# Performance work log

Hardware: AMD Instinct MI355X
Metric: run time of the kernel (lower is better)

## Reference

```python
import jax, jax.numpy as jnp
import numpy as np

N_NODES = 200_000
N_EDGES = 6_400_000
N_GRAPHS = 1024
F_IN = 16
H1 = 8
H2 = 16
STEPS = 4


def setup_inputs() -> dict:
    key = jax.random.key(0)
    ks = jax.random.split(key, 16)
    x = jax.random.normal(ks[0], (N_NODES, F_IN), jnp.float32)
    edge_index = jax.random.randint(ks[1], (2, N_EDGES), 0, N_NODES, dtype=jnp.int64)
    batch = jnp.sort(jax.random.randint(ks[2], (N_NODES,), 0, N_GRAPHS, dtype=jnp.int64))

    def p(k, shape):
        return jax.random.normal(k, shape, jnp.float32) * 0.1

    return {
        "x": x, "edge_index": edge_index, "batch": batch,
        # SAGEConv1: lin_l (neighbors, with bias) + lin_r (root, no bias)
        "W1l": p(ks[3], (H1, F_IN)), "b1l": jnp.zeros((H1,), jnp.float32), "W1r": p(ks[4], (H1, F_IN)),
        # SAGEConv2
        "W2l": p(ks[5], (H2, H1)), "b2l": jnp.zeros((H2,), jnp.float32), "W2r": p(ks[6], (H2, H1)),
        # Set2Set LSTM: input 2*H2, hidden H2, torch gate order (i, f, g, o)
        "Wih": p(ks[7], (4 * H2, 2 * H2)), "Whh": p(ks[8], (4 * H2, H2)),
        "bih": jnp.zeros((4 * H2,), jnp.float32), "bhh": jnp.zeros((4 * H2,), jnp.float32),
        # Final fc: 2*H2 -> 2
        "Wfc": p(ks[9], (2, 2 * H2)), "bfc": jnp.zeros((2,), jnp.float32),
    }


def _sage_conv(x, src, dst, Wl, bl, Wr):
    # PyG SAGEConv (mean aggr): out = lin_l(mean_j x_j) + lin_r(x_i)
    n = x.shape[0]
    agg = jax.ops.segment_sum(x[src], dst, num_segments=n)          # [N, F]
    deg = jax.ops.segment_sum(jnp.ones_like(dst, dtype=x.dtype), dst, num_segments=n)
    agg = agg / jnp.maximum(deg, 1.0)[:, None]
    return agg @ Wl.T + bl + x @ Wr.T


def _set2set(x, batch, Wih, Whh, bih, bhh):
    # order-invariant pooling with iterative content attention
    B = N_GRAPHS
    h = jnp.zeros((B, H2), x.dtype)
    c = jnp.zeros((B, H2), x.dtype)
    q_star = jnp.zeros((B, 2 * H2), x.dtype)
    for _ in range(STEPS):
        gates = q_star @ Wih.T + bih + h @ Whh.T + bhh
        i, f, g, o = jnp.split(gates, 4, axis=-1)
        c = jax.nn.sigmoid(f) * c + jax.nn.sigmoid(i) * jnp.tanh(g)
        h = jax.nn.sigmoid(o) * jnp.tanh(c)
        q = h                                                      # [B, H2]
        e = jnp.sum(x * q[batch], axis=-1)                         # [N]
        emax = jax.ops.segment_max(e, batch, num_segments=B)
        a = jnp.exp(e - emax[batch])
        asum = jax.ops.segment_sum(a, batch, num_segments=B)
        a = a / asum[batch]                                        # segment softmax
        r = jax.ops.segment_sum(a[:, None] * x, batch, num_segments=B)  # [B, H2]
        q_star = jnp.concatenate([q, r], axis=-1)
    return q_star


def reference(x, edge_index, batch, W1l, b1l, W1r, W2l, b2l, W2r,
              Wih, Whh, bih, bhh, Wfc, bfc):
    src, dst = edge_index[0], edge_index[1]
    x = jax.nn.relu(_sage_conv(x, src, dst, W1l, b1l, W1r))
    x = jax.nn.relu(_sage_conv(x, src, dst, W2l, b2l, W2r))
    q_star = _set2set(x, batch, Wih, Whh, bih, bhh)
    return q_star @ Wfc.T + bfc
```

## Files before the change

### kernel.cpp

```cpp
#include <hip/hip_runtime.h>

#define N_NODES 200000
#define N_EDGES 6400000
#define N_GRAPHS 1024
#define F_IN 16
#define H1 8
#define H2 16
#define STEPS 4

#define NB 1024
#define BNODES 196
#define CAPB 7168
#define CAP 7680
#define SMAX 320
#define RPT 14
#define RPADD 200

typedef _Float16 half8 __attribute__((ext_vector_type(8)));

__global__ void k_y1(const float* __restrict__ x, const float* __restrict__ W1l,
                     _Float16* __restrict__ y1) {
    int n = blockIdx.x * blockDim.x + threadIdx.x;
    if (n >= N_NODES) return;
    float xv[F_IN];
#pragma unroll
    for (int k = 0; k < F_IN; k++) xv[k] = x[(long long)n * F_IN + k];
    half8 o;
#pragma unroll
    for (int j = 0; j < H1; j++) {
        float s = 0.f;
#pragma unroll
        for (int k = 0; k < F_IN; k++) s += W1l[j * F_IN + k] * xv[k];
        o[j] = (_Float16)s;
    }
    *(half8*)&y1[(long long)n * H1] = o;
}

#define FILL_T 16384
__global__ __launch_bounds__(1024) void k_bin_fill(const int* __restrict__ src,
                                                   const int* __restrict__ dst,
                                                   int* __restrict__ gcur,
                                                   unsigned int* __restrict__ grec) {
    __shared__ int scnt[NB];
    __shared__ int soff[NB];
    int tid = threadIdx.x;
    long long ebase = (long long)blockIdx.x * FILL_T;
    scnt[tid] = 0;
    __syncthreads();
    unsigned int rec[16];
    unsigned int meta[16];
#pragma unroll
    for (int u = 0; u < 16; u++) {
        long long e = ebase + (long long)u * 1024 + tid;
        if (e < N_EDGES) {
            int d = __builtin_nontemporal_load(dst + e);
            int s = __builtin_nontemporal_load(src + e);
            int b = d / BNODES;
            int dl = d - b * BNODES;
            rec[u] = ((unsigned int)s << 8) | (unsigned int)dl;
            int r = atomicAdd(&scnt[b], 1);
            meta[u] = ((unsigned int)b << 16) | (unsigned int)r;
        } else {
            meta[u] = 0xFFFFFFFFu;
        }
    }
    __syncthreads();
    {
        int c = scnt[tid];
        soff[tid] = c ? atomicAdd(&gcur[tid], c) : 0;
    }
    __syncthreads();
#pragma unroll
    for (int u = 0; u < 16; u++) {
        if (meta[u] != 0xFFFFFFFFu) {
            int b = meta[u] >> 16;
            unsigned int slot = (unsigned int)soff[b] + (meta[u] & 0xFFFFu);
            if (slot < CAPB) grec[(unsigned int)b * CAPB + slot] = rec[u];
        }
    }
}

__device__ __forceinline__ void block_scan_hist(const int* hist, int* start,
                                                int tid, int* wsum) {
    int v = (tid < BNODES) ? hist[tid] : 0;
    int lane = tid & 63, w = tid >> 6;
    int s = v;
#pragma unroll
    for (int off = 1; off < 64; off <<= 1) {
        int u = __shfl_up(s, off);
        if (lane >= off) s += u;
    }
    if (lane == 63) wsum[w] = s;
    __syncthreads();
    int base = 0;
    for (int i = 0; i < w; i++) base += wsum[i];
    s += base;
    if (tid < BNODES) start[tid] = s - v;
    if (tid == 511) start[BNODES] = s;
    __syncthreads();
}

__global__ __launch_bounds__(512) void k_conv1(
    const float* __restrict__ x, const _Float16* __restrict__ y1,
    const int* __restrict__ bcount, unsigned int* __restrict__ grec,
    int* __restrict__ growptr,
    const float* __restrict__ b1l, const float* __restrict__ W1r,
    _Float16* __restrict__ h1) {
    __shared__ int lsrc[CAP];
    __shared__ int hist[BNODES];
    __shared__ int start[BNODES + 1];
    __shared__ int wsum[8];
    int b = blockIdx.x, tid = threadIdx.x;
    int rs = b * CAPB;
    int cnt = bcount[b]; if (cnt > CAPB) cnt = CAPB;
    for (int j = tid; j < BNODES; j += 512) hist[j] = 0;
    __syncthreads();
    unsigned int rec[RPT];
#pragma unroll
    for (int u = 0; u < RPT; u++) {
        int idx = u * 512 + tid;
        if (idx < cnt) {
            rec[u] = __builtin_nontemporal_load(grec + rs + idx);
            atomicAdd(&hist[rec[u] & 255], 1);
        } else {
            rec[u] = 0xFFFFFFFFu;
        }
    }
    __syncthreads();
    block_scan_hist(hist, start, tid, wsum);
    for (int j = tid; j < BNODES; j += 512) hist[j] = 0;
    __syncthreads();
#pragma unroll
    for (int u = 0; u < RPT; u++) {
        if (rec[u] != 0xFFFFFFFFu) {
            int dl = rec[u] & 255;
            int k = atomicAdd(&hist[dl], 1);
            lsrc[start[dl] + k] = (int)(rec[u] >> 8);
        }
    }
    __syncthreads();
    for (int j = tid; j < cnt; j += 512) grec[rs + j] = (unsigned int)lsrc[j];
    if (tid <= BNODES) growptr[b * RPADD + tid] = start[tid];
    if (tid < 2 * BNODES) {
        int dl = tid >> 1, half = tid & 1;
        int n = b * BNODES + dl;
        int s0 = start[dl], s1 = start[dl + 1];
        int mid = s0 + ((s1 - s0) >> 1);
        int ga = half ? mid : s0;
        int gb = half ? s1 : mid;
        float acc[H1];
#pragma unroll
        for (int k = 0; k < H1; k++) acc[k] = 0.f;
        int e = ga;
        for (; e + 4 <= gb; e += 4) {
            int a0 = lsrc[e], a1 = lsrc[e + 1], a2 = lsrc[e + 2], a3 = lsrc[e + 3];
            half8 v0 = *(const half8*)&y1[(long long)a0 * H1];
            half8 v1 = *(const half8*)&y1[(long long)a1 * H1];
            half8 v2 = *(const half8*)&y1[(long long)a2 * H1];
            half8 v3 = *(const half8*)&y1[(long long)a3 * H1];
#pragma unroll
            for (int k = 0; k < H1; k++)
                acc[k] += ((float)v0[k] + (float)v1[k]) + ((float)v2[k] + (float)v3[k]);
        }
        for (; e < gb; e++) {
            half8 v = *(const half8*)&y1[(long long)lsrc[e] * H1];
#pragma unroll
            for (int k = 0; k < H1; k++) acc[k] += (float)v[k];
        }
#pragma unroll
        for (int k = 0; k < H1; k++) acc[k] += __shfl_xor(acc[k], 1);
        if (half == 0 && n < N_NODES) {
            float inv = 1.0f / fmaxf((float)(s1 - s0), 1.0f);
            float xv[F_IN];
#pragma unroll
            for (int k = 0; k < F_IN; k++) xv[k] = x[(long long)n * F_IN + k];
            half8 o;
#pragma unroll
            for (int j = 0; j < H1; j++) {
                float s = acc[j] * inv + b1l[j];
#pragma unroll
                for (int k = 0; k < F_IN; k++) s += W1r[j * F_IN + k] * xv[k];
                o[j] = (_Float16)fmaxf(s, 0.0f);
            }
            *(half8*)&h1[(long long)n * H1] = o;
        }
    }
}

__global__ __launch_bounds__(512) void k_conv2(
    const _Float16* __restrict__ h1,
    const unsigned int* __restrict__ gsorted, const int* __restrict__ growptr,
    const float* __restrict__ b2l, const float* __restrict__ W2l,
    const float* __restrict__ W2r, float* __restrict__ h2) {
    int b = blockIdx.x, tid = threadIdx.x;
    if (tid >= 2 * BNODES) return;
    int dl = tid >> 1, half = tid & 1;
    int n = b * BNODES + dl;
    if (n >= N_NODES) return;
    int s0 = __builtin_nontemporal_load(growptr + b * RPADD + dl);
    int s1 = __builtin_nontemporal_load(growptr + b * RPADD + dl + 1);
    const unsigned int* seg = gsorted + (size_t)b * CAPB;
    int mid = s0 + ((s1 - s0) >> 1);
    int ga = half ? mid : s0;
    int gb = half ? s1 : mid;
    float acc[H1];
#pragma unroll
    for (int k = 0; k < H1; k++) acc[k] = 0.f;
    int e = ga;
    for (; e + 4 <= gb; e += 4) {
        int a0 = __builtin_nontemporal_load(seg + e);
        int a1 = __builtin_nontemporal_load(seg + e + 1);
        int a2 = __builtin_nontemporal_load(seg + e + 2);
        int a3 = __builtin_nontemporal_load(seg + e + 3);
        half8 v0 = *(const half8*)&h1[(long long)a0 * H1];
        half8 v1 = *(const half8*)&h1[(long long)a1 * H1];
        half8 v2 = *(const half8*)&h1[(long long)a2 * H1];
        half8 v3 = *(const half8*)&h1[(long long)a3 * H1];
#pragma unroll
        for (int k = 0; k < H1; k++)
            acc[k] += ((float)v0[k] + (float)v1[k]) + ((float)v2[k] + (float)v3[k]);
    }
    for (; e < gb; e++) {
        int a = __builtin_nontemporal_load(seg + e);
        half8 v = *(const half8*)&h1[(long long)a * H1];
#pragma unroll
        for (int k = 0; k < H1; k++) acc[k] += (float)v[k];
    }
#pragma unroll
    for (int k = 0; k < H1; k++) acc[k] += __shfl_xor(acc[k], 1);
    if (half == 0) {
        float inv = 1.0f / fmaxf((float)(s1 - s0), 1.0f);
        float av[H1], hv[H1];
        half8 hr = *(const half8*)&h1[(long long)n * H1];
#pragma unroll
        for (int k = 0; k < H1; k++) { hv[k] = (float)hr[k]; av[k] = acc[k] * inv; }
        float o[H2];
#pragma unroll
        for (int j = 0; j < H2; j++) {
            float s = b2l[j];
#pragma unroll
            for (int k = 0; k < H1; k++) s += W2l[j * H1 + k] * av[k] + W2r[j * H1 + k] * hv[k];
            o[j] = fmaxf(s, 0.0f);
        }
        *(float4*)&h2[(long long)n * H2] = make_float4(o[0], o[1], o[2], o[3]);
        *(float4*)&h2[(long long)n * H2 + 4] = make_float4(o[4], o[5], o[6], o[7]);
        *(float4*)&h2[(long long)n * H2 + 8] = make_float4(o[8], o[9], o[10], o[11]);
        *(float4*)&h2[(long long)n * H2 + 12] = make_float4(o[12], o[13], o[14], o[15]);
    }
}

__global__ void k_ptr(const int* __restrict__ batch, int* __restrict__ ptr) {
    int n = blockIdx.x * blockDim.x + threadIdx.x;
    if (n >= N_NODES) return;
    int b = batch[n];
    int bp = (n == 0) ? -1 : batch[n - 1];
    for (int g = bp + 1; g <= b; g++) ptr[g] = n;
    if (n == N_NODES - 1) {
        for (int g = b + 1; g <= N_GRAPHS; g++) ptr[g] = N_NODES;
    }
}

__global__ __launch_bounds__(256) void k_set2set(
    const float* __restrict__ h2, const int* __restrict__ ptr,
    const float* __restrict__ Wih, const float* __restrict__ Whh,
    const float* __restrict__ bih, const float* __restrict__ bhh,
    const float* __restrict__ Wfc, const float* __restrict__ bfc,
    float* __restrict__ out) {
    int b = blockIdx.x;
    int start = ptr[b], end = ptr[b + 1], cnt = end - start;
    __shared__ float sx[SMAX][H2 + 1];
    __shared__ float el[SMAX];
    __shared__ float sh[H2], sc[H2], sq[2 * H2], sg[4 * H2];
    __shared__ float red[4][17];
    __shared__ float s_emax, s_asum, s_r[H2];
    int tid = threadIdx.x;
    int wid = tid >> 6, lane = tid & 63;
    bool fit = (cnt <= SMAX);

    if (fit) {
        for (int i = start + tid; i < end; i += 256) {
            const float4* p = (const float4*)&h2[(long long)i * H2];
            float4 r0 = p[0], r1 = p[1], r2 = p[2], r3 = p[3];
            float* row = sx[i - start];
            row[0] = r0.x; row[1] = r0.y; row[2] = r0.z; row[3] = r0.w;
            row[4] = r1.x; row[5] = r1.y; row[6] = r1.z; row[7] = r1.w;
            row[8] = r2.x; row[9] = r2.y; row[10] = r2.z; row[11] = r2.w;
            row[12] = r3.x; row[13] = r3.y; row[14] = r3.z; row[15] = r3.w;
        }
    }
    if (tid < H2) { sh[tid] = 0.f; sc[tid] = 0.f; }
    if (tid < 2 * H2) sq[tid] = 0.f;
    __syncthreads();

    for (int step = 0; step < STEPS; step++) {
        if (tid < 64) {
            float g = bih[tid] + bhh[tid];
#pragma unroll
            for (int k = 0; k < 2 * H2; k++) g += Wih[tid * (2 * H2) + k] * sq[k];
#pragma unroll
            for (int k = 0; k < H2; k++) g += Whh[tid * H2 + k] * sh[k];
            sg[tid] = g;
        }
        __syncthreads();
        if (tid < H2) {
            float ig = 1.f / (1.f + expf(-sg[tid]));
            float fg = 1.f / (1.f + expf(-sg[H2 + tid]));
            float gg = tanhf(sg[2 * H2 + tid]);
            float og = 1.f / (1.f + expf(-sg[3 * H2 + tid]));
            float cc = fg * sc[tid] + ig * gg;
            sc[tid] = cc;
            sh[tid] = og * tanhf(cc);
        }
        __syncthreads();

        float lmax = -3.0e38f;
        if (fit) {
            for (int ii = tid; ii < cnt; ii += 256) {
                float e = 0.f;
#pragma unroll
                for (int k = 0; k < H2; k++) e += sx[ii][k] * sh[k];
                el[ii] = e;
                lmax = fmaxf(lmax, e);
            }
        } else {
            for (int i = start + tid; i < end; i += 256) {
                float e = 0.f;
#pragma unroll
                for (int k = 0; k < H2; k++) e += h2[(long long)i * H2 + k] * sh[k];
                lmax = fmaxf(lmax, e);
            }
        }
        for (int off = 32; off; off >>= 1) lmax = fmaxf(lmax, __shfl_down(lmax, off));
        if (lane == 0) red[wid][0] = lmax;
        __syncthreads();
        if (tid == 0) {
            float m = red[0][0];
            for (int w = 1; w < 4; w++) m = fmaxf(m, red[w][0]);
            s_emax = m;
        }
        __syncthreads();
        float emax = s_emax;

        float asum = 0.f, rloc[H2];
#pragma unroll
        for (int k = 0; k < H2; k++) rloc[k] = 0.f;
        if (fit) {
            for (int ii = tid; ii < cnt; ii += 256) {
                float a = expf(el[ii] - emax);
                asum += a;
#pragma unroll
                for (int k = 0; k < H2; k++) rloc[k] += a * sx[ii][k];
            }
        } else {
            for (int i = start + tid; i < end; i += 256) {
                float hv[H2];
                float e = 0.f;
#pragma unroll
                for (int k = 0; k < H2; k++) { hv[k] = h2[(long long)i * H2 + k]; e += hv[k] * sh[k]; }
                float a = expf(e - emax);
                asum += a;
#pragma unroll
                for (int k = 0; k < H2; k++) rloc[k] += a * hv[k];
            }
        }
        for (int off = 32; off; off >>= 1) {
            asum += __shfl_down(asum, off);
#pragma unroll
            for (int k = 0; k < H2; k++) rloc[k] += __shfl_down(rloc[k], off);
        }
        if (lane == 0) {
            red[wid][16] = asum;
#pragma unroll
            for (int k = 0; k < H2; k++) red[wid][k] = rloc[k];
        }
        __syncthreads();
        if (tid < 17) {
            float s = red[0][tid] + red[1][tid] + red[2][tid] + red[3][tid];
            if (tid == 16) s_asum = s; else s_r[tid] = s;
        }
        __syncthreads();
        if (tid < H2) {
            float rr = (cnt > 0 && s_asum > 0.f) ? s_r[tid] / s_asum : 0.0f;
            sq[tid] = sh[tid];
            sq[H2 + tid] = rr;
        }
        __syncthreads();
    }

    if (tid < 2) {
        float s = bfc[tid];
#pragma unroll
        for (int k = 0; k < 2 * H2; k++) s += Wfc[tid * (2 * H2) + k] * sq[k];
        out[b * 2 + tid] = s;
    }
}

extern "C" void kernel_launch(void* const* d_in, const int* in_sizes, int n_in,
                              void* d_out, int out_size, void* d_ws, size_t ws_size,
                              hipStream_t stream) {
    const float* x   = (const float*)d_in[0];
    const int*   ei  = (const int*)d_in[1];
    const int*   src = ei;
    const int*   dst = ei + N_EDGES;
    const int*   batch = (const int*)d_in[2];
    const float* W1l = (const float*)d_in[3];
    const float* b1l = (const float*)d_in[4];
    const float* W1r = (const float*)d_in[5];
    const float* W2l = (const float*)d_in[6];
    const float* b2l = (const float*)d_in[7];
    const float* W2r = (const float*)d_in[8];
    const float* Wih = (const float*)d_in[9];
    const float* Whh = (const float*)d_in[10];
    const float* bih = (const float*)d_in[11];
    const float* bhh = (const float*)d_in[12];
    const float* Wfc = (const float*)d_in[13];
    const float* bfc = (const float*)d_in[14];
    float* out = (float*)d_out;

    char* ws = (char*)d_ws;
    unsigned int* grec = (unsigned int*)ws;
    int* gcur = (int*)(grec + (size_t)NB * CAPB);
    int* growptr = gcur + NB;
    _Float16* y1 = (_Float16*)(growptr + (size_t)NB * RPADD);
    _Float16* h1 = y1 + (size_t)N_NODES * H1;
    float* h2  = (float*)(h1 + (size_t)N_NODES * H1);
    int*   ptr = (int*)(h2 + (size_t)N_NODES * H2);

    hipMemsetAsync(gcur, 0, (size_t)NB * sizeof(int), stream);

    int nb_node = (N_NODES + 255) / 256;
    int nb_fill = (int)(((long long)N_EDGES + FILL_T - 1) / FILL_T);

    k_y1<<<nb_node, 256, 0, stream>>>(x, W1l, y1);
    k_bin_fill<<<nb_fill, 1024, 0, stream>>>(src, dst, gcur, grec);
    k_conv1<<<NB, 512, 0, stream>>>(x, y1, gcur, grec, growptr, b1l, W1r, h1);
    k_conv2<<<NB, 512, 0, stream>>>(h1, grec, growptr, b2l, W2l, W2r, h2);
    k_ptr<<<nb_node, 256, 0, stream>>>(batch, ptr);
    k_set2set<<<N_GRAPHS, 256, 0, stream>>>(h2, ptr, Wih, Whh, bih, bhh, Wfc, bfc, out);
}
```

Baseline: 216.0 us.

## Split per-bin global edge cursors into eight slabs to cut atomic contention

```diff
diff --git a/kernel.cpp b/kernel.cpp
--- a/kernel.cpp
+++ b/kernel.cpp
@@ -10,10 +10,12 @@
 
 #define NB 1024
 #define BNODES 196
-#define CAPB 7168
+#define NSLAB 8
+#define CAPS 1024
+#define BSLOTS (NSLAB * CAPS)
 #define CAP 7680
 #define SMAX 320
-#define RPT 14
+#define RPT 16
 #define RPADD 200
 
 typedef _Float16 half8 __attribute__((ext_vector_type(8)));
@@ -39,11 +41,12 @@
 #define FILL_T 16384
 __global__ __launch_bounds__(1024) void k_bin_fill(const int* __restrict__ src,
                                                    const int* __restrict__ dst,
-                                                   int* __restrict__ gcur,
+                                                   int* __restrict__ gcur8,
                                                    unsigned int* __restrict__ grec) {
     __shared__ int scnt[NB];
     __shared__ int soff[NB];
     int tid = threadIdx.x;
+    int slab = blockIdx.x & (NSLAB - 1);
     long long ebase = (long long)blockIdx.x * FILL_T;
     scnt[tid] = 0;
     __syncthreads();
@@ -67,7 +70,7 @@
     __syncthreads();
     {
         int c = scnt[tid];
-        soff[tid] = c ? atomicAdd(&gcur[tid], c) : 0;
+        soff[tid] = c ? atomicAdd(&gcur8[tid * NSLAB + slab], c) : 0;
     }
     __syncthreads();
 #pragma unroll
@@ -75,7 +78,8 @@
         if (meta[u] != 0xFFFFFFFFu) {
             int b = meta[u] >> 16;
             unsigned int slot = (unsigned int)soff[b] + (meta[u] & 0xFFFFu);
-            if (slot < CAPB) grec[(unsigned int)b * CAPB + slot] = rec[u];
+            if (slot < CAPS)
+                grec[(size_t)b * BSLOTS + slab * CAPS + slot] = rec[u];
         }
     }
 }
@@ -102,7 +106,7 @@
 
 __global__ __launch_bounds__(512) void k_conv1(
     const float* __restrict__ x, const _Float16* __restrict__ y1,
-    const int* __restrict__ bcount, unsigned int* __restrict__ grec,
+    const int* __restrict__ gcur8, unsigned int* __restrict__ grec,
     int* __restrict__ growptr,
     const float* __restrict__ b1l, const float* __restrict__ W1r,
     _Float16* __restrict__ h1) {
@@ -110,17 +114,22 @@
     __shared__ int hist[BNODES];
     __shared__ int start[BNODES + 1];
     __shared__ int wsum[8];
+    __shared__ int cnt8[NSLAB];
     int b = blockIdx.x, tid = threadIdx.x;
-    int rs = b * CAPB;
-    int cnt = bcount[b]; if (cnt > CAPB) cnt = CAPB;
+    size_t base = (size_t)b * BSLOTS;
+    if (tid < NSLAB) {
+        int c = gcur8[b * NSLAB + tid];
+        cnt8[tid] = c > CAPS ? CAPS : c;
+    }
     for (int j = tid; j < BNODES; j += 512) hist[j] = 0;
     __syncthreads();
     unsigned int rec[RPT];
 #pragma unroll
     for (int u = 0; u < RPT; u++) {
         int idx = u * 512 + tid;
-        if (idx < cnt) {
-            rec[u] = __builtin_nontemporal_load(grec + rs + idx);
+        int s = idx >> 10, slot = idx & (CAPS - 1);
+        if (slot < cnt8[s]) {
+            rec[u] = __builtin_nontemporal_load(grec + base + idx);
             atomicAdd(&hist[rec[u] & 255], 1);
         } else {
             rec[u] = 0xFFFFFFFFu;
@@ -139,7 +148,9 @@
         }
     }
     __syncthreads();
-    for (int j = tid; j < cnt; j += 512) grec[rs + j] = (unsigned int)lsrc[j];
+    int total = start[BNODES];
+    for (int j = tid; j < total; j += 512)
+        __builtin_nontemporal_store((unsigned int)lsrc[j], grec + base + j);
     if (tid <= BNODES) growptr[b * RPADD + tid] = start[tid];
     if (tid < 2 * BNODES) {
         int dl = tid >> 1, half = tid & 1;
@@ -199,7 +210,7 @@
     if (n >= N_NODES) return;
     int s0 = __builtin_nontemporal_load(growptr + b * RPADD + dl);
     int s1 = __builtin_nontemporal_load(growptr + b * RPADD + dl + 1);
-    const unsigned int* seg = gsorted + (size_t)b * CAPB;
+    const unsigned int* seg = gsorted + (size_t)b * BSLOTS;
     int mid = s0 + ((s1 - s0) >> 1);
     int ga = half ? mid : s0;
     int gb = half ? s1 : mid;
@@ -419,21 +430,21 @@
 
     char* ws = (char*)d_ws;
     unsigned int* grec = (unsigned int*)ws;
-    int* gcur = (int*)(grec + (size_t)NB * CAPB);
-    int* growptr = gcur + NB;
+    int* gcur8 = (int*)(grec + (size_t)NB * BSLOTS);
+    int* growptr = gcur8 + NB * NSLAB;
     _Float16* y1 = (_Float16*)(growptr + (size_t)NB * RPADD);
     _Float16* h1 = y1 + (size_t)N_NODES * H1;
     float* h2  = (float*)(h1 + (size_t)N_NODES * H1);
     int*   ptr = (int*)(h2 + (size_t)N_NODES * H2);
 
-    hipMemsetAsync(gcur, 0, (size_t)NB * sizeof(int), stream);
+    hipMemsetAsync(gcur8, 0, (size_t)NB * NSLAB * sizeof(int), stream);
 
     int nb_node = (N_NODES + 255) / 256;
     int nb_fill = (int)(((long long)N_EDGES + FILL_T - 1) / FILL_T);
 
     k_y1<<<nb_node, 256, 0, stream>>>(x, W1l, y1);
-    k_bin_fill<<<nb_fill, 1024, 0, stream>>>(src, dst, gcur, grec);
-    k_conv1<<<NB, 512, 0, stream>>>(x, y1, gcur, grec, growptr, b1l, W1r, h1);
+    k_bin_fill<<<nb_fill, 1024, 0, stream>>>(src, dst, gcur8, grec);
+    k_conv1<<<NB, 512, 0, stream>>>(x, y1, gcur8, grec, growptr, b1l, W1r, h1);
     k_conv2<<<NB, 512, 0, stream>>>(h1, grec, growptr, b2l, W2l, W2r, h2);
     k_ptr<<<nb_node, 256, 0, stream>>>(batch, ptr);
     k_set2set<<<N_GRAPHS, 256, 0, stream>>>(h2, ptr, Wih, Whh, bih, bhh, Wfc, bfc, out);
```

Result: faster. 205.7 us (-4.7%).
